# Kernel optimization log

Hardware: AMD Instinct MI355X
Metric: run time of the kernel (lower is better)

Reference implementation:

```python
import jax, jax.numpy as jnp
import numpy as np

N, S, A, D = 2048, 4096, 4, 2


def setup_inputs() -> dict:
    key = jax.random.key(0)
    k1, k2 = jax.random.split(key, 2)
    # one-hot DNA sequences: tokens in [0, A)
    tokens_NxS = jax.random.randint(k1, (N, S), 0, A)
    data_NxSxA = jax.nn.one_hot(tokens_NxS, A, dtype=jnp.float32)
    # learnable per-sequence embedding table (EmbeddingTableSequenceEncoder)
    table_ND = jax.random.normal(k2, (N, D), dtype=jnp.float32) * 0.1
    # Hyperbolic distance learnable log-scale, initial scale 0.1
    log_scale = jnp.asarray(np.log(0.1), dtype=jnp.float32)
    return {"data_NxSxA": data_NxSxA, "table_ND": table_ND, "log_scale": log_scale}


def _hamming_NxN(data_NxSxA):
    # rows are one-hot, so per-site equality over A <=> dot product == 1
    s = jnp.float32(data_NxSxA.shape[1])
    matches_NxN = jnp.einsum("isa,jsa->ij", data_NxSxA, data_NxSxA)
    return (s - matches_NxN) / s


def _normalize(v_NxD):
    # softly clamp into the open unit ball via tanh on the norm
    norms_Nx1 = jnp.linalg.norm(v_NxD, axis=-1, keepdims=True)
    return v_NxD / jnp.maximum(norms_Nx1, 1e-12) * jnp.tanh(norms_Nx1)


def _hyperbolic_dist_NxN(table_ND, log_scale):
    z_ND = _normalize(table_ND)
    sq_norm_N = jnp.sum(z_ND * z_ND, axis=-1)            # ||z_i||^2
    diff_sq_NxN = jnp.sum((z_ND[:, None, :] - z_ND[None, :, :]) ** 2, axis=-1)
    denom_NxN = (1.0 - sq_norm_N)[:, None] * (1.0 - sq_norm_N)[None, :]
    arg_NxN = 1.0 + 2.0 * diff_sq_NxN / denom_NxN
    # clamp for numerical safety at the diagonal (arg == 1 exactly)
    dist_NxN = jnp.arccosh(jnp.maximum(arg_NxN, 1.0 + 1e-7))
    return dist_NxN * jnp.exp(log_scale)


def reference(data_NxSxA, table_ND, log_scale):
    hamming_NxN = _hamming_NxN(data_NxSxA)
    embed_NxN = _hyperbolic_dist_NxN(table_ND, log_scale)
    return jnp.mean((hamming_NxN - embed_NxN) ** 2)
```

## Files before the change

### kernel.cpp

```cpp
#include <hip/hip_runtime.h>

#define N_SEQ 2048
#define S_LEN 4096
#define W_SEQ 64
#define TILE 64
#define T_TILES (N_SEQ / TILE)
#define NBLK (T_TILES * (T_TILES + 1) / 2)
#define CHUNK 16
#define STRIDE 17
#define NSITES (N_SEQ * S_LEN)
#define ENC_BLOCKS 4096
#define ENC_THREADS (ENC_BLOCKS * 256)

typedef float vfloat4 __attribute__((ext_vector_type(4)));

__global__ __launch_bounds__(256) void encode_kernel(const vfloat4* __restrict__ data,
                                                     const float* __restrict__ table,
                                                     ulonglong2* __restrict__ codes,
                                                     float4* __restrict__ zbuf) {
    int tid = threadIdx.x;
    int gtid = blockIdx.x * 256 + tid;

    if (gtid < N_SEQ) {
        float vx = table[2 * gtid], vy = table[2 * gtid + 1];
        float n = sqrtf(vx * vx + vy * vy);
        float f = tanhf(n) / fmaxf(n, 1e-12f);
        float zx = vx * f, zy = vy * f;
        float omn = 1.0f - (zx * zx + zy * zy);
        zbuf[gtid] = make_float4(zx, zy, omn, 0.0f);
    }

#pragma unroll
    for (int it = 0; it < NSITES / ENC_THREADS; ++it) {
        int t = gtid + it * ENC_THREADS;
        vfloat4 v = __builtin_nontemporal_load(&data[t]);
        unsigned long long lo = __ballot(v.y + v.w > 0.5f);
        unsigned long long hi = __ballot(v.z + v.w > 0.5f);
        if ((tid & 63) == 0) {
            ulonglong2 e; e.x = lo; e.y = hi;
            codes[t >> 6] = e;
        }
    }
}

__global__ __launch_bounds__(256, 4) void pairs_kernel(const ulonglong2* __restrict__ codes,
                                                       const float4* __restrict__ zbuf,
                                                       const float* __restrict__ log_scale,
                                                       double* __restrict__ part) {
    __shared__ ulonglong2 As[TILE * STRIDE];
    __shared__ ulonglong2 Bs[TILE * STRIDE];
    __shared__ float wsum[4];

    int bid = blockIdx.x;
    int r = (int)((sqrtf(8.0f * (float)bid + 1.0f) - 1.0f) * 0.5f);
    while ((r + 1) * (r + 2) / 2 <= bid) ++r;
    while (r * (r + 1) / 2 > bid) --r;
    int c = bid - r * (r + 1) / 2;
    int i0 = c * TILE, j0 = r * TILE;

    int tid = threadIdx.x;
    int tx = tid & 15, ty = tid >> 4;

    int srow = tid >> 4, sw = tid & 15;
    const ulonglong2* gA = codes + (size_t)(i0 + srow) * W_SEQ + sw;
    const ulonglong2* gB = codes + (size_t)(j0 + srow) * W_SEQ + sw;
    ulonglong2* lA = As + srow * STRIDE + sw;
    ulonglong2* lB = Bs + srow * STRIDE + sw;

    int mis[4][4];
#pragma unroll
    for (int k = 0; k < 4; ++k)
#pragma unroll
        for (int l = 0; l < 4; ++l) mis[k][l] = 0;

    for (int cc = 0; cc < W_SEQ / CHUNK; ++cc) {
#pragma unroll
        for (int p = 0; p < 4; ++p) {
            lA[p * 16 * STRIDE] = gA[(size_t)(p * 16) * W_SEQ + cc * CHUNK];
            lB[p * 16 * STRIDE] = gB[(size_t)(p * 16) * W_SEQ + cc * CHUNK];
        }
        __syncthreads();
#pragma unroll
        for (int w = 0; w < CHUNK; ++w) {
            ulonglong2 a[4], bb[4];
#pragma unroll
            for (int k = 0; k < 4; ++k) a[k] = As[(ty + 16 * k) * STRIDE + w];
#pragma unroll
            for (int l = 0; l < 4; ++l) bb[l] = Bs[(tx + 16 * l) * STRIDE + w];
#pragma unroll
            for (int k = 0; k < 4; ++k)
#pragma unroll
                for (int l = 0; l < 4; ++l)
                    mis[k][l] += __popcll((a[k].x ^ bb[l].x) | (a[k].y ^ bb[l].y));
        }
        __syncthreads();
    }

    float scale = expf(log_scale[0]);
    const float inv_s = 1.0f / (float)S_LEN;
    float local = 0.0f;
#pragma unroll
    for (int k = 0; k < 4; ++k) {
        int i = i0 + ty + 16 * k;
        float4 zi = zbuf[i];
#pragma unroll
        for (int l = 0; l < 4; ++l) {
            int j = j0 + tx + 16 * l;
            float4 zj = zbuf[j];
            float ham = (float)mis[k][l] * inv_s;
            float dx = zi.x - zj.x, dy = zi.y - zj.y;
            float dsq = dx * dx + dy * dy;
            float arg = 1.0f + 2.0f * dsq / (zi.z * zj.z);
            arg = fmaxf(arg, 1.0f + 1e-7f);
            float dist = acoshf(arg) * scale;
            float d = ham - dist;
            float wgt = (i < j) ? 2.0f : (i == j ? 1.0f : 0.0f);
            local += wgt * d * d;
        }
    }

#pragma unroll
    for (int off = 32; off > 0; off >>= 1) local += __shfl_down(local, off);
    if ((tid & 63) == 0) wsum[tid >> 6] = local;
    __syncthreads();

    if (tid == 0)
        part[bid] = (double)(wsum[0] + wsum[1] + wsum[2] + wsum[3]);
}

__global__ __launch_bounds__(64) void reduce_kernel(const double* __restrict__ part,
                                                    float* __restrict__ out) {
    double s = 0.0;
    for (int i = threadIdx.x; i < NBLK; i += 64) s += part[i];
#pragma unroll
    for (int off = 32; off > 0; off >>= 1) s += __shfl_down(s, off);
    if (threadIdx.x == 0)
        out[0] = (float)(s / ((double)N_SEQ * (double)N_SEQ));
}

extern "C" void kernel_launch(void* const* d_in, const int* in_sizes, int n_in,
                              void* d_out, int out_size, void* d_ws, size_t ws_size,
                              hipStream_t stream) {
    const vfloat4* data     = (const vfloat4*)d_in[0];
    const float*  table     = (const float*)d_in[1];
    const float*  log_scale = (const float*)d_in[2];
    float* out = (float*)d_out;

    char* ws = (char*)d_ws;
    ulonglong2* codes   = (ulonglong2*)ws;
    float4*     zbuf    = (float4*)(ws + (size_t)N_SEQ * W_SEQ * sizeof(ulonglong2));
    double*     part    = (double*)((char*)zbuf + (size_t)N_SEQ * sizeof(float4));

    encode_kernel<<<ENC_BLOCKS, 256, 0, stream>>>(data, table, codes, zbuf);
    pairs_kernel <<<NBLK,       256, 0, stream>>>(codes, zbuf, log_scale, part);
    reduce_kernel<<<1,          64,  0, stream>>>(part, out);
}
```

Measured before the change: 245.4 us.

## Split pair-tile K dimension across two blocks and add separate epilogue kernel

```diff
diff --git a/kernel.cpp b/kernel.cpp
--- a/kernel.cpp
+++ b/kernel.cpp
@@ -5,7 +5,10 @@
 #define W_SEQ 64
 #define TILE 64
 #define T_TILES (N_SEQ / TILE)
-#define NBLK (T_TILES * (T_TILES + 1) / 2)
+#define NTILE (T_TILES * (T_TILES + 1) / 2)
+#define KSPLIT 2
+#define NBLK (NTILE * KSPLIT)
+#define KWORDS (W_SEQ / KSPLIT)
 #define CHUNK 16
 #define STRIDE 17
 #define NSITES (N_SEQ * S_LEN)
@@ -26,8 +29,7 @@
         float n = sqrtf(vx * vx + vy * vy);
         float f = tanhf(n) / fmaxf(n, 1e-12f);
         float zx = vx * f, zy = vy * f;
-        float omn = 1.0f - (zx * zx + zy * zy);
-        zbuf[gtid] = make_float4(zx, zy, omn, 0.0f);
+        zbuf[gtid] = make_float4(zx, zy, 1.0f - (zx * zx + zy * zy), 0.0f);
     }
 
 #pragma unroll
@@ -44,26 +46,25 @@
 }
 
 __global__ __launch_bounds__(256, 4) void pairs_kernel(const ulonglong2* __restrict__ codes,
-                                                       const float4* __restrict__ zbuf,
-                                                       const float* __restrict__ log_scale,
-                                                       double* __restrict__ part) {
+                                                       unsigned short* __restrict__ misbuf) {
     __shared__ ulonglong2 As[TILE * STRIDE];
     __shared__ ulonglong2 Bs[TILE * STRIDE];
-    __shared__ float wsum[4];
 
     int bid = blockIdx.x;
-    int r = (int)((sqrtf(8.0f * (float)bid + 1.0f) - 1.0f) * 0.5f);
-    while ((r + 1) * (r + 2) / 2 <= bid) ++r;
-    while (r * (r + 1) / 2 > bid) --r;
-    int c = bid - r * (r + 1) / 2;
+    int tb = bid >> 1, ko = bid & 1;
+    int r = (int)((sqrtf(8.0f * (float)tb + 1.0f) - 1.0f) * 0.5f);
+    while ((r + 1) * (r + 2) / 2 <= tb) ++r;
+    while (r * (r + 1) / 2 > tb) --r;
+    int c = tb - r * (r + 1) / 2;
     int i0 = c * TILE, j0 = r * TILE;
+    int w0 = ko * KWORDS;
 
     int tid = threadIdx.x;
     int tx = tid & 15, ty = tid >> 4;
 
     int srow = tid >> 4, sw = tid & 15;
-    const ulonglong2* gA = codes + (size_t)(i0 + srow) * W_SEQ + sw;
-    const ulonglong2* gB = codes + (size_t)(j0 + srow) * W_SEQ + sw;
+    const ulonglong2* gA = codes + (size_t)(i0 + srow) * W_SEQ + w0 + sw;
+    const ulonglong2* gB = codes + (size_t)(j0 + srow) * W_SEQ + w0 + sw;
     ulonglong2* lA = As + srow * STRIDE + sw;
     ulonglong2* lB = Bs + srow * STRIDE + sw;
 
@@ -73,7 +74,7 @@
 #pragma unroll
         for (int l = 0; l < 4; ++l) mis[k][l] = 0;
 
-    for (int cc = 0; cc < W_SEQ / CHUNK; ++cc) {
+    for (int cc = 0; cc < KWORDS / CHUNK; ++cc) {
 #pragma unroll
         for (int p = 0; p < 4; ++p) {
             lA[p * 16 * STRIDE] = gA[(size_t)(p * 16) * W_SEQ + cc * CHUNK];
@@ -96,18 +97,48 @@
         __syncthreads();
     }
 
+    unsigned short* mo = misbuf + (size_t)bid * (TILE * TILE);
+#pragma unroll
+    for (int k = 0; k < 4; ++k)
+#pragma unroll
+        for (int l = 0; l < 4; ++l)
+            mo[(ty + 16 * k) * TILE + tx + 16 * l] = (unsigned short)mis[k][l];
+}
+
+__global__ __launch_bounds__(256) void epi_kernel(const unsigned short* __restrict__ misbuf,
+                                                  const float4* __restrict__ zbuf,
+                                                  const float* __restrict__ log_scale,
+                                                  double* __restrict__ part) {
+    __shared__ float wsum[4];
+    int t = blockIdx.x;
+    int r = (int)((sqrtf(8.0f * (float)t + 1.0f) - 1.0f) * 0.5f);
+    while ((r + 1) * (r + 2) / 2 <= t) ++r;
+    while (r * (r + 1) / 2 > t) --r;
+    int c = t - r * (r + 1) / 2;
+    int i0 = c * TILE, j0 = r * TILE;
+
+    int tid = threadIdx.x;
+    int row = tid >> 2;
+    int c0  = (tid & 3) * 16;
+
+    const unsigned* m0 = (const unsigned*)(misbuf + (size_t)(2 * t) * (TILE * TILE)
+                                           + row * TILE + c0);
+    const unsigned* m1 = m0 + (TILE * TILE) / 2;
+
     float scale = expf(log_scale[0]);
     const float inv_s = 1.0f / (float)S_LEN;
+    int i = i0 + row;
+    float4 zi = zbuf[i];
     float local = 0.0f;
 #pragma unroll
-    for (int k = 0; k < 4; ++k) {
-        int i = i0 + ty + 16 * k;
-        float4 zi = zbuf[i];
+    for (int q = 0; q < 8; ++q) {
+        unsigned ua = m0[q], ub = m1[q];
 #pragma unroll
-        for (int l = 0; l < 4; ++l) {
-            int j = j0 + tx + 16 * l;
+        for (int h = 0; h < 2; ++h) {
+            int mtot = (int)((ua >> (16 * h)) & 0xffffu) + (int)((ub >> (16 * h)) & 0xffffu);
+            int j = j0 + c0 + 2 * q + h;
             float4 zj = zbuf[j];
-            float ham = (float)mis[k][l] * inv_s;
+            float ham = (float)mtot * inv_s;
             float dx = zi.x - zj.x, dy = zi.y - zj.y;
             float dsq = dx * dx + dy * dy;
             float arg = 1.0f + 2.0f * dsq / (zi.z * zj.z);
@@ -123,19 +154,23 @@
     for (int off = 32; off > 0; off >>= 1) local += __shfl_down(local, off);
     if ((tid & 63) == 0) wsum[tid >> 6] = local;
     __syncthreads();
-
     if (tid == 0)
-        part[bid] = (double)(wsum[0] + wsum[1] + wsum[2] + wsum[3]);
+        part[t] = (double)(wsum[0] + wsum[1] + wsum[2] + wsum[3]);
 }
 
-__global__ __launch_bounds__(64) void reduce_kernel(const double* __restrict__ part,
-                                                    float* __restrict__ out) {
+__global__ __launch_bounds__(256) void reduce_kernel(const double* __restrict__ part,
+                                                     float* __restrict__ out) {
+    __shared__ double ws[4];
+    int tid = threadIdx.x;
     double s = 0.0;
-    for (int i = threadIdx.x; i < NBLK; i += 64) s += part[i];
+    for (int i = tid; i < NTILE; i += 256) s += part[i];
 #pragma unroll
     for (int off = 32; off > 0; off >>= 1) s += __shfl_down(s, off);
-    if (threadIdx.x == 0)
-        out[0] = (float)(s / ((double)N_SEQ * (double)N_SEQ));
+    if ((tid & 63) == 0) ws[tid >> 6] = s;
+    __syncthreads();
+    if (tid == 0)
+        out[0] = (float)((ws[0] + ws[1] + ws[2] + ws[3]) /
+                         ((double)N_SEQ * (double)N_SEQ));
 }
 
 extern "C" void kernel_launch(void* const* d_in, const int* in_sizes, int n_in,
@@ -147,11 +182,14 @@
     float* out = (float*)d_out;
 
     char* ws = (char*)d_ws;
-    ulonglong2* codes   = (ulonglong2*)ws;
-    float4*     zbuf    = (float4*)(ws + (size_t)N_SEQ * W_SEQ * sizeof(ulonglong2));
-    double*     part    = (double*)((char*)zbuf + (size_t)N_SEQ * sizeof(float4));
+    ulonglong2*     codes  = (ulonglong2*)ws;
+    float4*         zbuf   = (float4*)(ws + (size_t)N_SEQ * W_SEQ * sizeof(ulonglong2));
+    unsigned short* misbuf = (unsigned short*)((char*)zbuf + (size_t)N_SEQ * sizeof(float4));
+    double*         part   = (double*)((char*)misbuf +
+                                       (size_t)NBLK * TILE * TILE * sizeof(unsigned short));
 
     encode_kernel<<<ENC_BLOCKS, 256, 0, stream>>>(data, table, codes, zbuf);
-    pairs_kernel <<<NBLK,       256, 0, stream>>>(codes, zbuf, log_scale, part);
-    reduce_kernel<<<1,          64,  0, stream>>>(part, out);
+    pairs_kernel <<<NBLK,       256, 0, stream>>>(codes, misbuf);
+    epi_kernel   <<<NTILE,      256, 0, stream>>>(misbuf, zbuf, log_scale, part);
+    reduce_kernel<<<1,          256, 0, stream>>>(part, out);
 }
```

After: 244.4 us. About the same (-0.4%).
